# Performance work log

Hardware: AMD Instinct MI355X
Metric: run time of the kernel (lower is better)

Reference implementation:

```python
import jax, jax.numpy as jnp
import numpy as np

T, N = 20, 32768          # seq_length, numNodes
D_IN, D_EMB, D_H, D_OUT = 2, 64, 128, 5


def setup_inputs() -> dict:
    key = jax.random.key(0)
    ks = jax.random.split(key, 12)
    s = 0.05
    return {
        "nodes": jax.random.normal(ks[0], (T, N, D_IN), jnp.float32),
        "present_mask": jax.random.randint(ks[1], (T, N), 0, 2).astype(bool),
        "hidden_states": jax.random.normal(ks[2], (N, D_H), jnp.float32),
        "cell_states": jax.random.normal(ks[3], (N, D_H), jnp.float32),
        "W_embed": jax.random.normal(ks[4], (D_IN, D_EMB), jnp.float32) * s,
        "b_embed": jnp.zeros((D_EMB,), jnp.float32),
        "W_ih": jax.random.normal(ks[5], (D_EMB, 4 * D_H), jnp.float32) * s,
        "b_ih": jnp.zeros((4 * D_H,), jnp.float32),
        "W_hh": jax.random.normal(ks[6], (D_H, 4 * D_H), jnp.float32) * s,
        "b_hh": jnp.zeros((4 * D_H,), jnp.float32),
        "W_out": jax.random.normal(ks[7], (D_H, D_OUT), jnp.float32) * s,
        "b_out": jnp.zeros((D_OUT,), jnp.float32),
    }


def reference(nodes, present_mask, hidden_states, cell_states,
              W_embed, b_embed, W_ih, b_ih, W_hh, b_hh, W_out, b_out):
    # Per-frame: gather present nodes -> embed+ReLU (dropout=eval identity)
    # -> LSTMCell -> scatter h/c/output back. Gather+scatter is expressed as
    # a masked update, which is mathematically identical.
    def step(carry, frame):
        h, c = carry
        x, mask = frame                      # x: [N,2], mask: [N]
        emb = jax.nn.relu(x @ W_embed + b_embed)              # [N,Demb]
        gates = emb @ W_ih + b_ih + h @ W_hh + b_hh           # [N,4H]
        i, f, g, o = jnp.split(gates, 4, axis=-1)             # torch order
        i, f, o = jax.nn.sigmoid(i), jax.nn.sigmoid(f), jax.nn.sigmoid(o)
        g = jnp.tanh(g)
        c_new = f * c + i * g
        h_new = o * jnp.tanh(c_new)
        m = mask[:, None]
        h = jnp.where(m, h_new, h)
        c = jnp.where(m, c_new, c)
        out = jnp.where(m, h_new @ W_out + b_out, 0.0)        # absent -> zeros
        return (h, c), out

    (h_fin, c_fin), outputs = jax.lax.scan(
        step, (hidden_states, cell_states), (nodes, present_mask))
    return outputs, h_fin, c_fin                              # [T,N,5],[N,H],[N,H]
```

## Files before the change

### kernel.cpp

```cpp
#include <hip/hip_runtime.h>
#include <cstddef>


typedef __attribute__((ext_vector_type(8))) short  s16x8;
typedef __attribute__((ext_vector_type(4))) float  f32x4;

namespace {
constexpr int T_STEPS = 20;
constexpr int NN      = 32768;
constexpr int D_EMB   = 64;
constexpr int D_H     = 128;
constexpr int D_OUT   = 5;
constexpr int G4      = 512;
constexpr int MT      = 64;
constexpr int BLOCK   = 512;
constexpr int GRID    = NN / MT;
constexpr int WP_ELEMS   = 8 * 4 * 6 * 64 * 8;
constexpr int WOUT_ELEMS = 4 * 64 * 8;
constexpr size_t OFF_H = (size_t)T_STEPS * NN * D_OUT;
constexpr size_t OFF_C = OFF_H + (size_t)NN * D_H;
}

__device__ __forceinline__ unsigned short f2bf(float x) {
    unsigned u = __float_as_uint(x);
    u = (u + 0x7FFFu + ((u >> 16) & 1u)) >> 16;
    return (unsigned short)u;
}
__device__ __forceinline__ float bf2f(unsigned short h) {
    return __uint_as_float(((unsigned)h) << 16);
}
__device__ __forceinline__ float sigf(float x) {
    return __builtin_amdgcn_rcpf(1.0f + __expf(-x));
}
__device__ __forceinline__ float tanhf_fast(float x) {
    return fmaf(-2.0f, __builtin_amdgcn_rcpf(1.0f + __expf(2.0f * x)), 1.0f);
}

__global__ void prepack_kernel(const float* __restrict__ W_ih,
                               const float* __restrict__ b_ih,
                               const float* __restrict__ W_hh,
                               const float* __restrict__ b_hh,
                               const float* __restrict__ W_out,
                               unsigned short* __restrict__ Wp,
                               unsigned short* __restrict__ WoutF,
                               float* __restrict__ b_sum) {
    int idx = blockIdx.x * blockDim.x + threadIdx.x;
    if (idx < WP_ELEMS) {
        int j    = idx & 7;
        int L    = (idx >> 3) & 63;
        int rest = idx >> 9;
        int kb   = rest % 6;
        int gw   = rest / 6;
        int g    = gw & 3, w = gw >> 2;
        int k    = kb * 32 + (L >> 4) * 8 + j;
        int col  = g * D_H + w * 16 + (L & 15);
        float v  = (k < D_EMB) ? W_ih[k * G4 + col] : W_hh[(k - D_EMB) * G4 + col];
        Wp[idx] = f2bf(v);
    } else if (idx < WP_ELEMS + WOUT_ELEMS) {
        int i2 = idx - WP_ELEMS;
        int j = i2 & 7, L = (i2 >> 3) & 63, kb2 = i2 >> 9;
        int k = kb2 * 32 + (L >> 4) * 8 + j;
        int n = L & 15;
        WoutF[i2] = (n < D_OUT) ? f2bf(W_out[k * D_OUT + n]) : (unsigned short)0;
    }
    if (idx < G4) b_sum[idx] = b_ih[idx] + b_hh[idx];
}

__global__ __launch_bounds__(BLOCK, 2) void vlstm_kernel(
    const float* __restrict__ nodes,
    const int*   __restrict__ mask,
    const float* __restrict__ h0,
    const float* __restrict__ c0,
    const float* __restrict__ W_embed,
    const float* __restrict__ b_embed,
    const float* __restrict__ b_out,
    const unsigned short* __restrict__ Wp,
    const unsigned short* __restrict__ WoutF,
    const float* __restrict__ b_sum,
    float* __restrict__ out)
{
    __shared__ __align__(16) unsigned short A[24 * 64 * 8];
    __shared__ __align__(16) float st_out[MT * D_OUT];
    __shared__ float We_s[2 * D_EMB];
    __shared__ float be_s[D_EMB];
    __shared__ int   msk_s[2][MT];

    const int tid  = threadIdx.x;
    const int wave = tid >> 6;
    const int L    = tid & 63;
    const int quad = L >> 4;
    const int l15  = L & 15;
    const int n_base = blockIdx.x * MT;

    const unsigned short* wbase = Wp + (size_t)wave * (4 * 6 * 64 * 8);
    s16x8 Bf[4][6];
    #pragma unroll
    for (int g = 0; g < 4; g++)
        #pragma unroll
        for (int kb = 0; kb < 6; kb++)
            Bf[g][kb] = *(const s16x8*)(wbase + ((g * 6 + kb) * 64 + L) * 8);
    s16x8 WoF[4];
    #pragma unroll
    for (int kb2 = 0; kb2 < 4; kb2++)
        WoF[kb2] = *(const s16x8*)(WoutF + ((kb2 * 64) + L) * 8);

    float bias[4];
    #pragma unroll
    for (int g = 0; g < 4; g++) bias[g] = b_sum[g * D_H + wave * 16 + l15];
    const float bo = (l15 < D_OUT) ? b_out[l15] : 0.0f;

    for (int i = tid; i < 3 * D_EMB; i += BLOCK) {
        if (i < 2 * D_EMB) We_s[i] = W_embed[i];
        else               be_s[i - 2 * D_EMB] = b_embed[i - 2 * D_EMB];
    }
    for (int i = tid; i < MT * D_H; i += BLOCK) {
        int node = i >> 7, u = i & 127;
        int k = D_EMB + u;
        int idx = (((node >> 4) * 6 + (k >> 5)) * 64 + ((k >> 3) & 3) * 16 + (node & 15)) * 8 + (k & 7);
        A[idx] = f2bf(h0[(size_t)(n_base + node) * D_H + u]);
    }
    const int u_lane = wave * 16 + l15;
    float c[4][4];
    #pragma unroll
    for (int rt = 0; rt < 4; rt++)
        #pragma unroll
        for (int r = 0; r < 4; r++) {
            int m = rt * 16 + quad * 4 + r;
            c[rt][r] = c0[(size_t)(n_base + m) * D_H + u_lane];
        }
    __syncthreads();

    const int node_e = tid >> 3;
    const int eb     = tid & 7;

    {
        const float2* xp = (const float2*)(nodes + ((size_t)0 * NN + n_base + node_e) * 2);
        float2 x = *xp;
        s16x8 ev;
        #pragma unroll
        for (int j = 0; j < 8; j++) {
            int e = eb * 8 + j;
            float v = fmaf(x.x, We_s[e], fmaf(x.y, We_s[D_EMB + e], be_s[e]));
            ev[j] = (short)f2bf(fmaxf(v, 0.0f));
        }
        int idx = (((node_e >> 4) * 6 + (eb >> 2)) * 64 + (eb & 3) * 16 + (node_e & 15)) * 8;
        *(s16x8*)(A + idx) = ev;
        if (tid < MT) msk_s[0][tid] = mask[(size_t)0 * NN + n_base + tid];
    }
    __syncthreads();

    for (int t = 0; t < T_STEPS; t++) {
        f32x4 acc[4][4];
        #pragma unroll
        for (int rt = 0; rt < 4; rt++)
            #pragma unroll
            for (int g = 0; g < 4; g++)
                acc[rt][g] = (f32x4){bias[g], bias[g], bias[g], bias[g]};
        #pragma unroll
        for (int kb = 0; kb < 6; kb++) {
            #pragma unroll
            for (int rt = 0; rt < 4; rt++) {
                s16x8 af = *(const s16x8*)(A + ((rt * 6 + kb) * 64 + L) * 8);
                #pragma unroll
                for (int g = 0; g < 4; g++)
                    acc[rt][g] = __builtin_amdgcn_mfma_f32_16x16x32_bf16(
                        af, Bf[g][kb], acc[rt][g], 0, 0, 0);
            }
        }

        unsigned mbits = 0;
        unsigned short hbf[4][4];
        #pragma unroll
        for (int rt = 0; rt < 4; rt++)
            #pragma unroll
            for (int r = 0; r < 4; r++) {
                int m = rt * 16 + quad * 4 + r;
                int mval = msk_s[t & 1][m];
                float gi = sigf(acc[rt][0][r]);
                float gf = sigf(acc[rt][1][r]);
                float gg = tanhf_fast(acc[rt][2][r]);
                float go = sigf(acc[rt][3][r]);
                float cn = fmaf(gf, c[rt][r], gi * gg);
                float hv = go * tanhf_fast(cn);
                if (mval) { c[rt][r] = cn; mbits |= 1u << (rt * 4 + r); }
                hbf[rt][r] = f2bf(hv);
            }
        __syncthreads();

        if (t > 0 && tid < MT * D_OUT)
            out[((size_t)(t - 1) * NN + n_base) * D_OUT + tid] = st_out[tid];

        {
            int kb_u = 2 + (u_lane >> 5);
            int fl   = ((u_lane >> 3) & 3) * 16 + quad * 4;
            int j_u  = u_lane & 7;
            #pragma unroll
            for (int rt = 0; rt < 4; rt++)
                #pragma unroll
                for (int r = 0; r < 4; r++)
                    if ((mbits >> (rt * 4 + r)) & 1u)
                        A[((rt * 6 + kb_u) * 64 + fl + r) * 8 + j_u] = hbf[rt][r];
        }
        if (t + 1 < T_STEPS) {
            const float2* xp = (const float2*)(nodes + ((size_t)(t + 1) * NN + n_base + node_e) * 2);
            float2 x = *xp;
            s16x8 ev;
            #pragma unroll
            for (int j = 0; j < 8; j++) {
                int e = eb * 8 + j;
                float v = fmaf(x.x, We_s[e], fmaf(x.y, We_s[D_EMB + e], be_s[e]));
                ev[j] = (short)f2bf(fmaxf(v, 0.0f));
            }
            int idx = (((node_e >> 4) * 6 + (eb >> 2)) * 64 + (eb & 3) * 16 + (node_e & 15)) * 8;
            *(s16x8*)(A + idx) = ev;
            if (tid < MT) msk_s[(t + 1) & 1][tid] = mask[(size_t)(t + 1) * NN + n_base + tid];
        }
        __syncthreads();

        if (wave < 4) {
            const int rt = wave;
            f32x4 ao = (f32x4){0.0f, 0.0f, 0.0f, 0.0f};
            #pragma unroll
            for (int kb2 = 0; kb2 < 4; kb2++) {
                s16x8 af = *(const s16x8*)(A + ((rt * 6 + 2 + kb2) * 64 + L) * 8);
                ao = __builtin_amdgcn_mfma_f32_16x16x32_bf16(af, WoF[kb2], ao, 0, 0, 0);
            }
            if (l15 < D_OUT) {
                #pragma unroll
                for (int r = 0; r < 4; r++) {
                    int node = rt * 16 + quad * 4 + r;
                    int mv = msk_s[t & 1][node];
                    st_out[node * D_OUT + l15] = mv ? (ao[r] + bo) : 0.0f;
                }
            }
        }
    }

    __syncthreads();
    if (tid < MT * D_OUT)
        out[((size_t)(T_STEPS - 1) * NN + n_base) * D_OUT + tid] = st_out[tid];

    for (int i = tid; i < MT * D_H; i += BLOCK) {
        int node = i >> 7, u = i & 127;
        int k = D_EMB + u;
        int idx = (((node >> 4) * 6 + (k >> 5)) * 64 + ((k >> 3) & 3) * 16 + (node & 15)) * 8 + (k & 7);
        out[OFF_H + (size_t)(n_base + node) * D_H + u] = bf2f(A[idx]);
    }
    #pragma unroll
    for (int rt = 0; rt < 4; rt++)
        #pragma unroll
        for (int r = 0; r < 4; r++) {
            int m = rt * 16 + quad * 4 + r;
            out[OFF_C + (size_t)(n_base + m) * D_H + u_lane] = c[rt][r];
        }
}

extern "C" void kernel_launch(void* const* d_in, const int* in_sizes, int n_in,
                              void* d_out, int out_size, void* d_ws, size_t ws_size,
                              hipStream_t stream) {
    const float* nodes   = (const float*)d_in[0];
    const int*   mask    = (const int*)  d_in[1];
    const float* h0      = (const float*)d_in[2];
    const float* c0      = (const float*)d_in[3];
    const float* W_embed = (const float*)d_in[4];
    const float* b_embed = (const float*)d_in[5];
    const float* W_ih    = (const float*)d_in[6];
    const float* b_ih    = (const float*)d_in[7];
    const float* W_hh    = (const float*)d_in[8];
    const float* b_hh    = (const float*)d_in[9];
    const float* W_out   = (const float*)d_in[10];
    const float* b_out   = (const float*)d_in[11];
    float* out = (float*)d_out;

    unsigned short* Wp    = (unsigned short*)d_ws;
    unsigned short* WoutF = Wp + WP_ELEMS;
    float*          b_sum = (float*)(WoutF + WOUT_ELEMS);

    prepack_kernel<<<(WP_ELEMS + WOUT_ELEMS + 255) / 256, 256, 0, stream>>>(
        W_ih, b_ih, W_hh, b_hh, W_out, Wp, WoutF, b_sum);

    vlstm_kernel<<<GRID, BLOCK, 0, stream>>>(
        nodes, mask, h0, c0, W_embed, b_embed, b_out, Wp, WoutF, b_sum, out);
}
```

Measured before the change: 330.6 us.

## Double-buffer the LDS operand tile to drop a barrier per LSTM step

The shared A tile (embedding plus hidden state) and the output staging buffer are now double-buffered. New h and the next step's embedding go into the alternate buffer, which removes one __syncthreads per timestep. The next step's x and mask loads are issued before the gate MFMAs to hide global latency. Hidden state is kept in registers and written straight to the output, float-to-bf16 conversion uses the hardware cast, and output stores are vectorized to 16 bytes. The cost is double the LDS footprint for A, which could limit occupancy.

Measured after the change: 340.6 us. 3.0% more time.

```diff
diff --git a/kernel.cpp b/kernel.cpp
--- a/kernel.cpp
+++ b/kernel.cpp
@@ -17,6 +17,7 @@
 constexpr int GRID    = NN / MT;
 constexpr int WP_ELEMS   = 8 * 4 * 6 * 64 * 8;
 constexpr int WOUT_ELEMS = 4 * 64 * 8;
+constexpr int A_ELEMS    = 24 * 64 * 8;
 constexpr size_t OFF_H = (size_t)T_STEPS * NN * D_OUT;
 constexpr size_t OFF_C = OFF_H + (size_t)NN * D_H;
 }
@@ -25,6 +26,12 @@
     unsigned u = __float_as_uint(x);
     u = (u + 0x7FFFu + ((u >> 16) & 1u)) >> 16;
     return (unsigned short)u;
+}
+__device__ __forceinline__ unsigned short f2bf_hw(float x) {
+    __bf16 b = (__bf16)x;
+    union { __bf16 b; unsigned short u; } cv;
+    cv.b = b;
+    return cv.u;
 }
 __device__ __forceinline__ float bf2f(unsigned short h) {
     return __uint_as_float(((unsigned)h) << 16);
@@ -79,8 +86,8 @@
     const float* __restrict__ b_sum,
     float* __restrict__ out)
 {
-    __shared__ __align__(16) unsigned short A[24 * 64 * 8];
-    __shared__ __align__(16) float st_out[MT * D_OUT];
+    __shared__ __align__(16) unsigned short A[2][A_ELEMS];
+    __shared__ __align__(16) float st_out[2][MT * D_OUT];
     __shared__ float We_s[2 * D_EMB];
     __shared__ float be_s[D_EMB];
     __shared__ int   msk_s[2][MT];
@@ -104,35 +111,36 @@
     for (int kb2 = 0; kb2 < 4; kb2++)
         WoF[kb2] = *(const s16x8*)(WoutF + ((kb2 * 64) + L) * 8);
 
+    const int u_lane = wave * 16 + l15;
     float bias[4];
     #pragma unroll
     for (int g = 0; g < 4; g++) bias[g] = b_sum[g * D_H + wave * 16 + l15];
     const float bo = (l15 < D_OUT) ? b_out[l15] : 0.0f;
+
+    const int kb_u = 2 + (u_lane >> 5);
+    const int fl   = ((u_lane >> 3) & 3) * 16 + quad * 4;
+    const int j_u  = u_lane & 7;
 
     for (int i = tid; i < 3 * D_EMB; i += BLOCK) {
         if (i < 2 * D_EMB) We_s[i] = W_embed[i];
         else               be_s[i - 2 * D_EMB] = b_embed[i - 2 * D_EMB];
     }
-    for (int i = tid; i < MT * D_H; i += BLOCK) {
-        int node = i >> 7, u = i & 127;
-        int k = D_EMB + u;
-        int idx = (((node >> 4) * 6 + (k >> 5)) * 64 + ((k >> 3) & 3) * 16 + (node & 15)) * 8 + (k & 7);
-        A[idx] = f2bf(h0[(size_t)(n_base + node) * D_H + u]);
-    }
-    const int u_lane = wave * 16 + l15;
-    float c[4][4];
+
+    float          c[4][4];
+    unsigned short hr[4][4];
     #pragma unroll
     for (int rt = 0; rt < 4; rt++)
         #pragma unroll
         for (int r = 0; r < 4; r++) {
             int m = rt * 16 + quad * 4 + r;
-            c[rt][r] = c0[(size_t)(n_base + m) * D_H + u_lane];
-        }
-    __syncthreads();
+            c[rt][r]  = c0[(size_t)(n_base + m) * D_H + u_lane];
+            hr[rt][r] = f2bf_hw(h0[(size_t)(n_base + m) * D_H + u_lane]);
+            A[0][((rt * 6 + kb_u) * 64 + fl + r) * 8 + j_u] = hr[rt][r];
+        }
 
     const int node_e = tid >> 3;
     const int eb     = tid & 7;
-
+    const int idx_e  = (((node_e >> 4) * 6 + (eb >> 2)) * 64 + (eb & 3) * 16 + (node_e & 15)) * 8;
     {
         const float2* xp = (const float2*)(nodes + ((size_t)0 * NN + n_base + node_e) * 2);
         float2 x = *xp;
@@ -141,15 +149,24 @@
         for (int j = 0; j < 8; j++) {
             int e = eb * 8 + j;
             float v = fmaf(x.x, We_s[e], fmaf(x.y, We_s[D_EMB + e], be_s[e]));
-            ev[j] = (short)f2bf(fmaxf(v, 0.0f));
-        }
-        int idx = (((node_e >> 4) * 6 + (eb >> 2)) * 64 + (eb & 3) * 16 + (node_e & 15)) * 8;
-        *(s16x8*)(A + idx) = ev;
+            ev[j] = (short)f2bf_hw(fmaxf(v, 0.0f));
+        }
+        *(s16x8*)(&A[0][idx_e]) = ev;
         if (tid < MT) msk_s[0][tid] = mask[(size_t)0 * NN + n_base + tid];
     }
     __syncthreads();
 
     for (int t = 0; t < T_STEPS; t++) {
+        unsigned short* __restrict__ Ar = A[t & 1];
+        unsigned short* __restrict__ Aw = A[(t + 1) & 1];
+
+        float2 xv = make_float2(0.0f, 0.0f);
+        int    lm = 0;
+        if (t + 1 < T_STEPS) {
+            xv = *(const float2*)(nodes + ((size_t)(t + 1) * NN + n_base + node_e) * 2);
+            if (tid < MT) lm = mask[(size_t)(t + 1) * NN + n_base + tid];
+        }
+
         f32x4 acc[4][4];
         #pragma unroll
         for (int rt = 0; rt < 4; rt++)
@@ -160,7 +177,7 @@
         for (int kb = 0; kb < 6; kb++) {
             #pragma unroll
             for (int rt = 0; rt < 4; rt++) {
-                s16x8 af = *(const s16x8*)(A + ((rt * 6 + kb) * 64 + L) * 8);
+                s16x8 af = *(const s16x8*)(Ar + ((rt * 6 + kb) * 64 + L) * 8);
                 #pragma unroll
                 for (int g = 0; g < 4; g++)
                     acc[rt][g] = __builtin_amdgcn_mfma_f32_16x16x32_bf16(
@@ -169,7 +186,6 @@
         }
 
         unsigned mbits = 0;
-        unsigned short hbf[4][4];
         #pragma unroll
         for (int rt = 0; rt < 4; rt++)
             #pragma unroll
@@ -182,75 +198,58 @@
                 float go = sigf(acc[rt][3][r]);
                 float cn = fmaf(gf, c[rt][r], gi * gg);
                 float hv = go * tanhf_fast(cn);
-                if (mval) { c[rt][r] = cn; mbits |= 1u << (rt * 4 + r); }
-                hbf[rt][r] = f2bf(hv);
-            }
-        __syncthreads();
-
-        if (t > 0 && tid < MT * D_OUT)
-            out[((size_t)(t - 1) * NN + n_base) * D_OUT + tid] = st_out[tid];
-
-        {
-            int kb_u = 2 + (u_lane >> 5);
-            int fl   = ((u_lane >> 3) & 3) * 16 + quad * 4;
-            int j_u  = u_lane & 7;
-            #pragma unroll
-            for (int rt = 0; rt < 4; rt++)
-                #pragma unroll
-                for (int r = 0; r < 4; r++)
-                    if ((mbits >> (rt * 4 + r)) & 1u)
-                        A[((rt * 6 + kb_u) * 64 + fl + r) * 8 + j_u] = hbf[rt][r];
-        }
+                unsigned short hb = f2bf_hw(hv);
+                if (mval) { c[rt][r] = cn; hr[rt][r] = hb; mbits |= 1u << (rt * 4 + r); }
+                Aw[((rt * 6 + kb_u) * 64 + fl + r) * 8 + j_u] = hr[rt][r];
+            }
+
         if (t + 1 < T_STEPS) {
-            const float2* xp = (const float2*)(nodes + ((size_t)(t + 1) * NN + n_base + node_e) * 2);
-            float2 x = *xp;
             s16x8 ev;
             #pragma unroll
             for (int j = 0; j < 8; j++) {
                 int e = eb * 8 + j;
-                float v = fmaf(x.x, We_s[e], fmaf(x.y, We_s[D_EMB + e], be_s[e]));
-                ev[j] = (short)f2bf(fmaxf(v, 0.0f));
-            }
-            int idx = (((node_e >> 4) * 6 + (eb >> 2)) * 64 + (eb & 3) * 16 + (node_e & 15)) * 8;
-            *(s16x8*)(A + idx) = ev;
-            if (tid < MT) msk_s[(t + 1) & 1][tid] = mask[(size_t)(t + 1) * NN + n_base + tid];
-        }
+                float v = fmaf(xv.x, We_s[e], fmaf(xv.y, We_s[D_EMB + e], be_s[e]));
+                ev[j] = (short)f2bf_hw(fmaxf(v, 0.0f));
+            }
+            *(s16x8*)(Aw + idx_e) = ev;
+            if (tid < MT) msk_s[(t + 1) & 1][tid] = lm;
+        }
+
         __syncthreads();
 
+        if (t > 0 && tid < MT * D_OUT / 4)
+            ((f32x4*)(out + ((size_t)(t - 1) * NN + n_base) * D_OUT))[tid] =
+                ((const f32x4*)st_out[(t - 1) & 1])[tid];
+
         if (wave < 4) {
-            const int rt = wave;
             f32x4 ao = (f32x4){0.0f, 0.0f, 0.0f, 0.0f};
             #pragma unroll
             for (int kb2 = 0; kb2 < 4; kb2++) {
-                s16x8 af = *(const s16x8*)(A + ((rt * 6 + 2 + kb2) * 64 + L) * 8);
+                s16x8 af = *(const s16x8*)(Aw + ((wave * 6 + 2 + kb2) * 64 + L) * 8);
                 ao = __builtin_amdgcn_mfma_f32_16x16x32_bf16(af, WoF[kb2], ao, 0, 0, 0);
             }
             if (l15 < D_OUT) {
                 #pragma unroll
                 for (int r = 0; r < 4; r++) {
-                    int node = rt * 16 + quad * 4 + r;
-                    int mv = msk_s[t & 1][node];
-                    st_out[node * D_OUT + l15] = mv ? (ao[r] + bo) : 0.0f;
+                    int node = wave * 16 + quad * 4 + r;
+                    int mv = (mbits >> (wave * 4 + r)) & 1u;
+                    st_out[t & 1][node * D_OUT + l15] = mv ? (ao[r] + bo) : 0.0f;
                 }
             }
         }
     }
 
     __syncthreads();
-    if (tid < MT * D_OUT)
-        out[((size_t)(T_STEPS - 1) * NN + n_base) * D_OUT + tid] = st_out[tid];
-
-    for (int i = tid; i < MT * D_H; i += BLOCK) {
-        int node = i >> 7, u = i & 127;
-        int k = D_EMB + u;
-        int idx = (((node >> 4) * 6 + (k >> 5)) * 64 + ((k >> 3) & 3) * 16 + (node & 15)) * 8 + (k & 7);
-        out[OFF_H + (size_t)(n_base + node) * D_H + u] = bf2f(A[idx]);
-    }
+    if (tid < MT * D_OUT / 4)
+        ((f32x4*)(out + ((size_t)(T_STEPS - 1) * NN + n_base) * D_OUT))[tid] =
+            ((const f32x4*)st_out[(T_STEPS - 1) & 1])[tid];
+
     #pragma unroll
     for (int rt = 0; rt < 4; rt++)
         #pragma unroll
         for (int r = 0; r < 4; r++) {
             int m = rt * 16 + quad * 4 + r;
+            out[OFF_H + (size_t)(n_base + m) * D_H + u_lane] = bf2f(hr[rt][r]);
             out[OFF_C + (size_t)(n_base + m) * D_H + u_lane] = c[rt][r];
         }
 }
```
